# Kernel tuning notes

Measured on AMD Instinct MI355X. Metric: run time of the kernel, lower is better.

## Reference

```python
import jax, jax.numpy as jnp
import numpy as np

B, C, H, W = 8, 64, 64, 64
MID = C // 8  # = 8, single-head key/query dim


def setup_inputs() -> dict:
    key = jax.random.key(0)
    ks = jax.random.split(key, 8)
    return {
        "x": jax.random.normal(ks[0], (B, C, H, W), dtype=jnp.float32),
        "wq": jax.random.normal(ks[1], (MID, C), dtype=jnp.float32) * 0.1,
        "bq": jax.random.normal(ks[2], (MID,), dtype=jnp.float32) * 0.1,
        "wk": jax.random.normal(ks[3], (MID, C), dtype=jnp.float32) * 0.1,
        "bk": jax.random.normal(ks[4], (MID,), dtype=jnp.float32) * 0.1,
        "wv": jax.random.normal(ks[5], (C, C), dtype=jnp.float32) * 0.1,
        "bv": jax.random.normal(ks[6], (C,), dtype=jnp.float32) * 0.1,
        "gamma": jax.random.uniform(ks[7], (1,), dtype=jnp.float32),
    }


def reference(x, wq, bq, wk, bk, wv, bv, gamma):
    b, c, h, w = x.shape
    n = h * w
    xf = x.reshape(b, c, n)  # [B, C, N]
    # 1x1 convs == per-pixel linear projections
    q = jnp.einsum("mc,bcn->bmn", wq, xf) + bq[:, None]  # [B, MID, N]
    k = jnp.einsum("mc,bcn->bmn", wk, xf) + bk[:, None]  # [B, MID, N]
    v = jnp.einsum("dc,bcn->bdn", wv, xf) + bv[:, None]  # [B, C, N]
    # attn[b, i, j] = softmax_j( q[:, i] . k[:, j] )  -- no scaling (SAGAN)
    attn = jax.nn.softmax(jnp.einsum("bmi,bmj->bij", q, k), axis=-1)  # [B, N, N]
    # out[b, c, i] = sum_j v[b, c, j] * attn[b, i, j]
    out = jnp.einsum("bcj,bij->bci", v, attn).reshape(b, c, h, w)
    return x + gamma[0] * out
```

## Files before the change

### kernel.cpp

```cpp
#include <hip/hip_runtime.h>
#include <math.h>

#define NB 8
#define NC 64
#define NN 4096
#define PS 72
#define SHIFTC 20.0f

typedef __attribute__((ext_vector_type(8))) short short8;
typedef __attribute__((ext_vector_type(4))) float float4v;

__device__ inline unsigned short f2bf(float f) {
    unsigned int u = __builtin_bit_cast(unsigned int, f);
    unsigned int r = (u + 0x7FFFu + ((u >> 16) & 1u)) >> 16;
    return (unsigned short)r;
}
__device__ inline unsigned int bfpack(float lo, float hi) {
    unsigned int a = __builtin_bit_cast(unsigned int, lo) + 0x8000u;
    unsigned int b = __builtin_bit_cast(unsigned int, hi) + 0x8000u;
    return __builtin_amdgcn_perm(b, a, 0x07060302u);
}

__global__ __launch_bounds__(256) void proj_mfma_kernel(
    const float* __restrict__ x,
    const float* __restrict__ wq, const float* __restrict__ bq,
    const float* __restrict__ wk, const float* __restrict__ bk,
    const float* __restrict__ wv, const float* __restrict__ bv,
    unsigned short* __restrict__ qo8, unsigned short* __restrict__ ko8,
    unsigned short* __restrict__ vo)
{
    const int b = blockIdx.y;
    const int wave = threadIdx.x >> 6, lane = threadIdx.x & 63;
    const int c0 = lane & 15, quad = lane >> 4;
    const int n0 = blockIdx.x * 64 + wave * 16;

    __shared__ unsigned short qkb[4][16][24];

    const float* xb = x + (size_t)b * NC * NN + n0 + c0;
    short8 xf[2];
#pragma unroll
    for (int kc = 0; kc < 2; ++kc)
#pragma unroll
        for (int e = 0; e < 8; ++e)
            xf[kc][e] = (short)f2bf(xb[(size_t)(kc * 32 + quad * 8 + e) * NN]);

#pragma unroll
    for (int mt = 0; mt < 4; ++mt) {
        short8 wf0, wf1;
#pragma unroll
        for (int e = 0; e < 8; ++e) {
            wf0[e] = (short)f2bf(wv[(mt * 16 + c0) * 64 + quad * 8 + e]);
            wf1[e] = (short)f2bf(wv[(mt * 16 + c0) * 64 + 32 + quad * 8 + e]);
        }
        float4v acc = {0.f, 0.f, 0.f, 0.f};
        acc = __builtin_amdgcn_mfma_f32_16x16x32_bf16(wf0, xf[0], acc, 0, 0, 0);
        acc = __builtin_amdgcn_mfma_f32_16x16x32_bf16(wf1, xf[1], acc, 0, 0, 0);
#pragma unroll
        for (int reg = 0; reg < 4; ++reg) {
            int ch = mt * 16 + quad * 4 + reg;
            vo[((size_t)b * NC + ch) * NN + n0 + c0] = f2bf(acc[reg] + bv[ch]);
        }
    }

    {
        const float* wrow = (c0 < 8) ? (wq + c0 * 64) : (wk + (c0 - 8) * 64);
        short8 wf0, wf1;
#pragma unroll
        for (int e = 0; e < 8; ++e) {
            wf0[e] = (short)f2bf(wrow[quad * 8 + e]);
            wf1[e] = (short)f2bf(wrow[32 + quad * 8 + e]);
        }
        float4v acc = {0.f, 0.f, 0.f, 0.f};
        acc = __builtin_amdgcn_mfma_f32_16x16x32_bf16(wf0, xf[0], acc, 0, 0, 0);
        acc = __builtin_amdgcn_mfma_f32_16x16x32_bf16(wf1, xf[1], acc, 0, 0, 0);
        float a[4];
#pragma unroll
        for (int reg = 0; reg < 4; ++reg) {
            int qr = quad * 4 + reg;
            float bias = (qr < 8) ? bq[qr] : bk[qr - 8];
            a[reg] = acc[reg] + bias;
        }
        *(uint2*)&qkb[wave][c0][quad * 4] = make_uint2(bfpack(a[0], a[1]), bfpack(a[2], a[3]));
        if (quad == 0) {
            uint4 qrow = *(const uint4*)&qkb[wave][c0][0];
            uint4 krow = *(const uint4*)&qkb[wave][c0][8];
            *(uint4*)&qo8[((size_t)b * NN + n0 + c0) * 8] = qrow;
            *(uint4*)&ko8[((size_t)b * NN + n0 + c0) * 8] = krow;
        }
    }
}

__global__ __launch_bounds__(256, 4) void attn_fused_kernel(
    const unsigned short* __restrict__ qo8, const unsigned short* __restrict__ ko8,
    const unsigned short* __restrict__ vo,
    const float* __restrict__ x, const float* __restrict__ gamma,
    float* __restrict__ out)
{
    const int b = blockIdx.y;
    const int i0b = blockIdx.x * 32;
    const int wave = threadIdx.x >> 6, lane = threadIdx.x & 63;
    const int c0 = lane & 15, quad = lane >> 4;

    __shared__ __align__(16) float obuf[4][32][65];
    __shared__ float lbuf[4][2][16];

    unsigned short* psw = (unsigned short*)obuf + wave * 16 * PS;
    unsigned short* pswr = psw + c0 * PS + quad * 4;
    const unsigned short* psrd = psw + c0 * PS + quad * 8;

    const int jbase = wave * (NN / 4);

    short8 qf[2] = {};
    if (quad == 0) {
        qf[0] = *(const short8*)(qo8 + ((size_t)b * NN + i0b + c0) * 8);
        qf[1] = *(const short8*)(qo8 + ((size_t)b * NN + i0b + 16 + c0) * 8);
    }

    float4v acc[2][4];
#pragma unroll
    for (int qh = 0; qh < 2; ++qh)
#pragma unroll
        for (int ct = 0; ct < 4; ++ct) acc[qh][ct] = (float4v){0.f, 0.f, 0.f, 0.f};
    float lsum[2] = {0.f, 0.f};

    const unsigned short* vbase = vo + ((size_t)b * NC + c0) * NN + jbase + quad * 8;
    const unsigned short* kbase = ko8 + ((size_t)(b * NN + jbase + c0)) * 8;

    for (int t = 0; t < NN / 4 / 64; ++t) {
        const int jt = t * 64;
        short8 kf[4] = {};
        if (quad == 0) {
#pragma unroll
            for (int st = 0; st < 4; ++st)
                kf[st] = *(const short8*)(kbase + (size_t)(jt + st * 16) * 8);
        }
        short8 vf[4][2];
#pragma unroll
        for (int ct = 0; ct < 4; ++ct)
#pragma unroll
            for (int kc = 0; kc < 2; ++kc)
                vf[ct][kc] = *(const short8*)(vbase + (size_t)ct * 16 * NN + jt + kc * 32);

#pragma unroll
        for (int qh = 0; qh < 2; ++qh) {
            float4v s[4];
#pragma unroll
            for (int st = 0; st < 4; ++st) {
                float4v z = {0.f, 0.f, 0.f, 0.f};
                s[st] = __builtin_amdgcn_mfma_f32_16x16x32_bf16(kf[st], qf[qh], z, 0, 0, 0);
            }
#pragma unroll
            for (int st = 0; st < 4; ++st) {
                float p0 = __expf(s[st][0] - SHIFTC);
                float p1 = __expf(s[st][1] - SHIFTC);
                float p2 = __expf(s[st][2] - SHIFTC);
                float p3 = __expf(s[st][3] - SHIFTC);
                lsum[qh] += (p0 + p1) + (p2 + p3);
                *(uint2*)(pswr + st * 16) = make_uint2(bfpack(p0, p1), bfpack(p2, p3));
            }
#pragma unroll
            for (int kc = 0; kc < 2; ++kc) {
                short8 pf = *(const short8*)(psrd + kc * 32);
#pragma unroll
                for (int ct = 0; ct < 4; ++ct)
                    acc[qh][ct] = __builtin_amdgcn_mfma_f32_16x16x32_bf16(
                        pf, vf[ct][kc], acc[qh][ct], 0, 0, 0);
            }
        }
    }

#pragma unroll
    for (int qh = 0; qh < 2; ++qh) {
        lsum[qh] += __shfl_xor(lsum[qh], 16);
        lsum[qh] += __shfl_xor(lsum[qh], 32);
    }

    __syncthreads();

    if (quad == 0) {
        lbuf[wave][0][c0] = lsum[0];
        lbuf[wave][1][c0] = lsum[1];
    }
#pragma unroll
    for (int qh = 0; qh < 2; ++qh)
#pragma unroll
        for (int ct = 0; ct < 4; ++ct)
#pragma unroll
            for (int reg = 0; reg < 4; ++reg)
                obuf[wave][qh * 16 + quad * 4 + reg][ct * 16 + c0] = acc[qh][ct][reg];
    __syncthreads();

    const int q = threadIdx.x & 31;
    const int cg = threadIdx.x >> 5;
    const float L = lbuf[0][q >> 4][q & 15] + lbuf[1][q >> 4][q & 15] +
                    lbuf[2][q >> 4][q & 15] + lbuf[3][q >> 4][q & 15];
    const float scale = gamma[0] / L;
    const size_t base = (size_t)b * NC * NN + i0b + q;
#pragma unroll
    for (int cc = 0; cc < 8; ++cc) {
        const int ch = cg * 8 + cc;
        const float O = obuf[0][q][ch] + obuf[1][q][ch] + obuf[2][q][ch] + obuf[3][q][ch];
        const size_t idx = base + (size_t)ch * NN;
        out[idx] = x[idx] + scale * O;
    }
}

extern "C" void kernel_launch(void* const* d_in, const int* in_sizes, int n_in,
                              void* d_out, int out_size, void* d_ws, size_t ws_size,
                              hipStream_t stream) {
    const float* x     = (const float*)d_in[0];
    const float* wq    = (const float*)d_in[1];
    const float* bq    = (const float*)d_in[2];
    const float* wk    = (const float*)d_in[3];
    const float* bk    = (const float*)d_in[4];
    const float* wv    = (const float*)d_in[5];
    const float* bv    = (const float*)d_in[6];
    const float* gamma = (const float*)d_in[7];
    float* out = (float*)d_out;

    unsigned short* wss = (unsigned short*)d_ws;
    unsigned short* qo8 = wss;
    unsigned short* ko8 = qo8 + (size_t)NB * NN * 8;
    unsigned short* vo  = ko8 + (size_t)NB * NN * 8;

    proj_mfma_kernel<<<dim3(NN / 64, NB), 256, 0, stream>>>(
        x, wq, bq, wk, bk, wv, bv, qo8, ko8, vo);
    attn_fused_kernel<<<dim3(NN / 32, NB), 256, 0, stream>>>(
        qo8, ko8, vo, x, gamma, out);
}
```

Before: 146.9 us.

## Keep softmax probabilities in registers via permlane32 swap instead of LDS round-trip

The P tile no longer goes through LDS. Probabilities are packed with the hardware bf16 convert and rearranged across lanes with permlane32_swap so they fit the MFMA B-operand layout. To make that work, the projection kernel writes V columns in a permuted pixel order, the -SHIFT offset is folded into the MFMA accumulator init, and per-wave output partials are combined with LDS atomicAdd into one smaller buffer. This removes the per-tile LDS store and load of P and shrinks shared memory, at the cost of inline asm, an extra zero-init pass and a barrier, and LDS atomics in the epilogue.

```diff
diff --git a/kernel.cpp b/kernel.cpp
--- a/kernel.cpp
+++ b/kernel.cpp
@@ -4,11 +4,12 @@
 #define NB 8
 #define NC 64
 #define NN 4096
-#define PS 72
 #define SHIFTC 20.0f
 
 typedef __attribute__((ext_vector_type(8))) short short8;
 typedef __attribute__((ext_vector_type(4))) float float4v;
+typedef __attribute__((ext_vector_type(4))) unsigned int uint4v;
+typedef __attribute__((ext_vector_type(2))) int int2v;
 
 __device__ inline unsigned short f2bf(float f) {
     unsigned int u = __builtin_bit_cast(unsigned int, f);
@@ -19,6 +20,16 @@
     unsigned int a = __builtin_bit_cast(unsigned int, lo) + 0x8000u;
     unsigned int b = __builtin_bit_cast(unsigned int, hi) + 0x8000u;
     return __builtin_amdgcn_perm(b, a, 0x07060302u);
+}
+__device__ inline unsigned int cvtpk(float lo, float hi) {
+    unsigned int r;
+    asm("v_cvt_pk_bf16_f32 %0, %1, %2" : "=v"(r) : "v"(lo), "v"(hi));
+    return r;
+}
+__device__ inline void plswap(unsigned int& x, unsigned int& y) {
+    int2v r = __builtin_amdgcn_permlane32_swap((int)x, (int)y, false, false);
+    x = (unsigned int)r[0];
+    y = (unsigned int)r[1];
 }
 
 __global__ __launch_bounds__(256) void proj_mfma_kernel(
@@ -44,6 +55,8 @@
         for (int e = 0; e < 8; ++e)
             xf[kc][e] = (short)f2bf(xb[(size_t)(kc * 32 + quad * 8 + e) * NN]);
 
+    const int c0p = (c0 & 3) | ((c0 & 8) >> 1) | ((c0 & 4) << 1);
+
 #pragma unroll
     for (int mt = 0; mt < 4; ++mt) {
         short8 wf0, wf1;
@@ -58,7 +71,7 @@
 #pragma unroll
         for (int reg = 0; reg < 4; ++reg) {
             int ch = mt * 16 + quad * 4 + reg;
-            vo[((size_t)b * NC + ch) * NN + n0 + c0] = f2bf(acc[reg] + bv[ch]);
+            vo[((size_t)b * NC + ch) * NN + n0 + c0p] = f2bf(acc[reg] + bv[ch]);
         }
     }
 
@@ -101,12 +114,12 @@
     const int wave = threadIdx.x >> 6, lane = threadIdx.x & 63;
     const int c0 = lane & 15, quad = lane >> 4;
 
-    __shared__ __align__(16) float obuf[4][32][65];
+    __shared__ __align__(16) float oacc[32][65];
     __shared__ float lbuf[4][2][16];
 
-    unsigned short* psw = (unsigned short*)obuf + wave * 16 * PS;
-    unsigned short* pswr = psw + c0 * PS + quad * 4;
-    const unsigned short* psrd = psw + c0 * PS + quad * 8;
+    for (int i = threadIdx.x; i < 32 * 65; i += 256)
+        ((float*)oacc)[i] = 0.f;
+    __syncthreads();
 
     const int jbase = wave * (NN / 4);
 
@@ -143,29 +156,43 @@
 
 #pragma unroll
         for (int qh = 0; qh < 2; ++qh) {
+            const float4v mC = {-SHIFTC, -SHIFTC, -SHIFTC, -SHIFTC};
             float4v s[4];
 #pragma unroll
+            for (int st = 0; st < 4; ++st)
+                s[st] = __builtin_amdgcn_mfma_f32_16x16x32_bf16(kf[st], qf[qh], mC, 0, 0, 0);
+
+            unsigned int D[4][2];
+            float ls = 0.f;
+#pragma unroll
             for (int st = 0; st < 4; ++st) {
-                float4v z = {0.f, 0.f, 0.f, 0.f};
-                s[st] = __builtin_amdgcn_mfma_f32_16x16x32_bf16(kf[st], qf[qh], z, 0, 0, 0);
+                float p0 = __expf(s[st][0]);
+                float p1 = __expf(s[st][1]);
+                float p2 = __expf(s[st][2]);
+                float p3 = __expf(s[st][3]);
+                ls += (p0 + p1) + (p2 + p3);
+                D[st][0] = cvtpk(p0, p1);
+                D[st][1] = cvtpk(p2, p3);
             }
-#pragma unroll
-            for (int st = 0; st < 4; ++st) {
-                float p0 = __expf(s[st][0] - SHIFTC);
-                float p1 = __expf(s[st][1] - SHIFTC);
-                float p2 = __expf(s[st][2] - SHIFTC);
-                float p3 = __expf(s[st][3] - SHIFTC);
-                lsum[qh] += (p0 + p1) + (p2 + p3);
-                *(uint2*)(pswr + st * 16) = make_uint2(bfpack(p0, p1), bfpack(p2, p3));
-            }
-#pragma unroll
-            for (int kc = 0; kc < 2; ++kc) {
-                short8 pf = *(const short8*)(psrd + kc * 32);
-#pragma unroll
-                for (int ct = 0; ct < 4; ++ct)
-                    acc[qh][ct] = __builtin_amdgcn_mfma_f32_16x16x32_bf16(
-                        pf, vf[ct][kc], acc[qh][ct], 0, 0, 0);
-            }
+            lsum[qh] += ls;
+
+            unsigned int a00 = D[0][0], b00 = D[1][0];  plswap(a00, b00);
+            unsigned int a01 = D[0][1], b01 = D[1][1];  plswap(a01, b01);
+            unsigned int a10 = D[2][0], b10 = D[3][0];  plswap(a10, b10);
+            unsigned int a11 = D[2][1], b11 = D[3][1];  plswap(a11, b11);
+            uint4v u0 = {a00, a01, b00, b01};
+            uint4v u1 = {a10, a11, b10, b11};
+            short8 pf0 = __builtin_bit_cast(short8, u0);
+            short8 pf1 = __builtin_bit_cast(short8, u1);
+
+#pragma unroll
+            for (int ct = 0; ct < 4; ++ct)
+                acc[qh][ct] = __builtin_amdgcn_mfma_f32_16x16x32_bf16(
+                    pf0, vf[ct][0], acc[qh][ct], 0, 0, 0);
+#pragma unroll
+            for (int ct = 0; ct < 4; ++ct)
+                acc[qh][ct] = __builtin_amdgcn_mfma_f32_16x16x32_bf16(
+                    pf1, vf[ct][1], acc[qh][ct], 0, 0, 0);
         }
     }
 
@@ -174,20 +201,18 @@
         lsum[qh] += __shfl_xor(lsum[qh], 16);
         lsum[qh] += __shfl_xor(lsum[qh], 32);
     }
-
-    __syncthreads();
-
     if (quad == 0) {
         lbuf[wave][0][c0] = lsum[0];
         lbuf[wave][1][c0] = lsum[1];
     }
+
 #pragma unroll
     for (int qh = 0; qh < 2; ++qh)
 #pragma unroll
         for (int ct = 0; ct < 4; ++ct)
 #pragma unroll
             for (int reg = 0; reg < 4; ++reg)
-                obuf[wave][qh * 16 + quad * 4 + reg][ct * 16 + c0] = acc[qh][ct][reg];
+                atomicAdd(&oacc[qh * 16 + quad * 4 + reg][ct * 16 + c0], acc[qh][ct][reg]);
     __syncthreads();
 
     const int q = threadIdx.x & 31;
@@ -199,7 +224,7 @@
 #pragma unroll
     for (int cc = 0; cc < 8; ++cc) {
         const int ch = cg * 8 + cc;
-        const float O = obuf[0][q][ch] + obuf[1][q][ch] + obuf[2][q][ch] + obuf[3][q][ch];
+        const float O = oacc[q][ch];
         const size_t idx = base + (size_t)ch * NN;
         out[idx] = x[idx] + scale * O;
     }
```

Measured after the change: 163.2 us. 11.1% more time.

## Split attention key range across two blocks and combine partials in separate kernel

Applied to the files above, without the earlier changes.

Splits the key/value sequence into two halves via a third grid dimension, doubling the number of attention blocks, and writes bf16 partial outputs and row sums to workspace. A new combine kernel adds the two partials, normalizes, and applies the residual. The per-wave output reduction now uses shared-memory atomics into a single buffer instead of four separate buffers, which lowers LDS use. The cost is extra global traffic for the partials, an added kernel launch, and bf16 rounding of the partial outputs.

```diff
diff --git a/kernel.cpp b/kernel.cpp
--- a/kernel.cpp
+++ b/kernel.cpp
@@ -14,6 +14,9 @@
     unsigned int u = __builtin_bit_cast(unsigned int, f);
     unsigned int r = (u + 0x7FFFu + ((u >> 16) & 1u)) >> 16;
     return (unsigned short)r;
+}
+__device__ inline float bf2f(unsigned int lo16) {
+    return __builtin_bit_cast(float, lo16 << 16);
 }
 __device__ inline unsigned int bfpack(float lo, float hi) {
     unsigned int a = __builtin_bit_cast(unsigned int, lo) + 0x8000u;
@@ -93,22 +96,27 @@
 __global__ __launch_bounds__(256, 4) void attn_fused_kernel(
     const unsigned short* __restrict__ qo8, const unsigned short* __restrict__ ko8,
     const unsigned short* __restrict__ vo,
-    const float* __restrict__ x, const float* __restrict__ gamma,
-    float* __restrict__ out)
+    unsigned short* __restrict__ po, float* __restrict__ pl)
 {
     const int b = blockIdx.y;
     const int i0b = blockIdx.x * 32;
+    const int jh = blockIdx.z;
     const int wave = threadIdx.x >> 6, lane = threadIdx.x & 63;
     const int c0 = lane & 15, quad = lane >> 4;
 
-    __shared__ __align__(16) float obuf[4][32][65];
+    __shared__ unsigned short ps[4][16][PS];
+    __shared__ __align__(16) float oacc[32][65];
     __shared__ float lbuf[4][2][16];
 
-    unsigned short* psw = (unsigned short*)obuf + wave * 16 * PS;
+    for (int i = threadIdx.x; i < 32 * 65; i += 256)
+        ((float*)oacc)[i] = 0.f;
+    __syncthreads();
+
+    unsigned short* psw = &ps[wave][0][0];
     unsigned short* pswr = psw + c0 * PS + quad * 4;
     const unsigned short* psrd = psw + c0 * PS + quad * 8;
 
-    const int jbase = wave * (NN / 4);
+    const int jbase = jh * (NN / 2) + wave * (NN / 8);
 
     short8 qf[2] = {};
     if (quad == 0) {
@@ -126,7 +134,7 @@
     const unsigned short* vbase = vo + ((size_t)b * NC + c0) * NN + jbase + quad * 8;
     const unsigned short* kbase = ko8 + ((size_t)(b * NN + jbase + c0)) * 8;
 
-    for (int t = 0; t < NN / 4 / 64; ++t) {
+    for (int t = 0; t < NN / 8 / 64; ++t) {
         const int jt = t * 64;
         short8 kf[4] = {};
         if (quad == 0) {
@@ -174,35 +182,58 @@
         lsum[qh] += __shfl_xor(lsum[qh], 16);
         lsum[qh] += __shfl_xor(lsum[qh], 32);
     }
-
-    __syncthreads();
-
     if (quad == 0) {
         lbuf[wave][0][c0] = lsum[0];
         lbuf[wave][1][c0] = lsum[1];
     }
+
 #pragma unroll
     for (int qh = 0; qh < 2; ++qh)
 #pragma unroll
         for (int ct = 0; ct < 4; ++ct)
 #pragma unroll
             for (int reg = 0; reg < 4; ++reg)
-                obuf[wave][qh * 16 + quad * 4 + reg][ct * 16 + c0] = acc[qh][ct][reg];
+                atomicAdd(&oacc[qh * 16 + quad * 4 + reg][ct * 16 + c0], acc[qh][ct][reg]);
     __syncthreads();
 
     const int q = threadIdx.x & 31;
     const int cg = threadIdx.x >> 5;
     const float L = lbuf[0][q >> 4][q & 15] + lbuf[1][q >> 4][q & 15] +
                     lbuf[2][q >> 4][q & 15] + lbuf[3][q >> 4][q & 15];
-    const float scale = gamma[0] / L;
-    const size_t base = (size_t)b * NC * NN + i0b + q;
+    unsigned short* poh = po + (size_t)jh * NB * NC * NN;
+    float* plh = pl + (size_t)jh * NB * NN;
+    if (cg == 0) plh[(size_t)b * NN + i0b + q] = L;
 #pragma unroll
     for (int cc = 0; cc < 8; ++cc) {
         const int ch = cg * 8 + cc;
-        const float O = obuf[0][q][ch] + obuf[1][q][ch] + obuf[2][q][ch] + obuf[3][q][ch];
-        const size_t idx = base + (size_t)ch * NN;
-        out[idx] = x[idx] + scale * O;
-    }
+        poh[((size_t)b * NC + ch) * NN + i0b + q] = f2bf(oacc[q][ch]);
+    }
+}
+
+__global__ __launch_bounds__(256) void combine_kernel(
+    const unsigned short* __restrict__ po, const float* __restrict__ pl,
+    const float* __restrict__ x, const float* __restrict__ gamma,
+    float* __restrict__ out)
+{
+    const size_t H = (size_t)NB * NC * NN;
+    const size_t i4 = ((size_t)blockIdx.x * 256 + threadIdx.x) * 4;
+    const int n  = (int)(i4 % NN);
+    const int bc = (int)(i4 / NN);
+    const int b  = bc >> 6;
+
+    uint2 u0 = *(const uint2*)(po + (size_t)bc * NN + n);
+    uint2 u1 = *(const uint2*)(po + H + (size_t)bc * NN + n);
+    float4 l0 = *(const float4*)(pl + (size_t)b * NN + n);
+    float4 l1 = *(const float4*)(pl + (size_t)NB * NN + (size_t)b * NN + n);
+    float4 xv = *(const float4*)(x + i4);
+    const float g = gamma[0];
+
+    float4 ov;
+    ov.x = xv.x + g * (bf2f(u0.x & 0xffffu) + bf2f(u1.x & 0xffffu)) / (l0.x + l1.x);
+    ov.y = xv.y + g * (bf2f(u0.x >> 16)     + bf2f(u1.x >> 16))     / (l0.y + l1.y);
+    ov.z = xv.z + g * (bf2f(u0.y & 0xffffu) + bf2f(u1.y & 0xffffu)) / (l0.z + l1.z);
+    ov.w = xv.w + g * (bf2f(u0.y >> 16)     + bf2f(u1.y >> 16))     / (l0.w + l1.w);
+    *(float4*)(out + i4) = ov;
 }
 
 extern "C" void kernel_launch(void* const* d_in, const int* in_sizes, int n_in,
@@ -222,9 +253,13 @@
     unsigned short* qo8 = wss;
     unsigned short* ko8 = qo8 + (size_t)NB * NN * 8;
     unsigned short* vo  = ko8 + (size_t)NB * NN * 8;
+    unsigned short* po  = vo  + (size_t)NB * NC * NN;
+    float* pl = (float*)(po + 2 * (size_t)NB * NC * NN);
 
     proj_mfma_kernel<<<dim3(NN / 64, NB), 256, 0, stream>>>(
         x, wq, bq, wk, bk, wv, bv, qo8, ko8, vo);
-    attn_fused_kernel<<<dim3(NN / 32, NB), 256, 0, stream>>>(
-        qo8, ko8, vo, x, gamma, out);
-}
+    attn_fused_kernel<<<dim3(NN / 32, NB, 2), 256, 0, stream>>>(
+        qo8, ko8, vo, po, pl);
+    combine_kernel<<<dim3(NB * NC * NN / 4 / 256), 256, 0, stream>>>(
+        po, pl, x, gamma, out);
+}
```

After: 219.5 us. +49.5%, slower.
